# Kernel optimization log

Hardware: AMD Instinct MI355X
Metric: run time of the kernel (lower is better)

The kernel has to match this reference:

```python
import jax, jax.numpy as jnp
import numpy as np

N, E = 100000, 1600000
NFEAT, H2, H3, H4, NCLASS = 512, 256, 256, 128, 16


def setup_inputs() -> dict:
    key = jax.random.key(0)
    ks = jax.random.split(key, 12)
    def glorot(k, shape):
        fan_in = shape[0]
        return jax.random.normal(k, shape, dtype=jnp.float32) * (1.0 / np.sqrt(fan_in))
    return {
        "x": jax.random.normal(ks[0], (N, NFEAT), dtype=jnp.float32),
        "edge_row": jax.random.randint(ks[1], (E,), 0, N, dtype=jnp.int32),
        "edge_col": jax.random.randint(ks[2], (E,), 0, N, dtype=jnp.int32),
        # positive weights ~ normalized adjacency values (scale ~1/avg_degree)
        "edge_val": jax.random.uniform(ks[3], (E,), dtype=jnp.float32) * (1.0 / 16.0),
        "W1": glorot(ks[4], (NFEAT, H2)), "b1": jnp.zeros((H2,), jnp.float32),
        "W2": glorot(ks[5], (H2, H3)),   "b2": jnp.zeros((H3,), jnp.float32),
        "W3": glorot(ks[6], (H3, H4)),   "b3": jnp.zeros((H4,), jnp.float32),
        "Wd": glorot(ks[7], (H4, NCLASS)), "bd": jnp.zeros((NCLASS,), jnp.float32),
    }


def reference(x, edge_row, edge_col, edge_val, W1, b1, W2, b2, W3, b3, Wd, bd):
    n = x.shape[0]

    def spmm(h):
        # adj @ h with adj in COO form: out[row] += val * h[col]
        return jax.ops.segment_sum(edge_val[:, None] * h[edge_col], edge_row, num_segments=n)

    # gc1 -> relu -> (dropout is identity in eval) -> gc2 -> relu -> gc3 -> relu -> dense
    h = jax.nn.relu(spmm(x @ W1) + b1)
    h = jax.nn.relu(spmm(h @ W2) + b2)
    h = jax.nn.relu(spmm(h @ W3) + b3)
    return h @ Wd + bd
```

## Files before the change

### kernel.cpp

```cpp
#include <hip/hip_runtime.h>
#include <hip/hip_bf16.h>
#include <cstdint>
#include <cstddef>

#define NFEAT 512
#define H2 256
#define H3 256
#define H4 128
#define NCLASS 16

typedef __attribute__((ext_vector_type(8))) short short8;
typedef __attribute__((ext_vector_type(4))) float f32x4;
typedef __attribute__((ext_vector_type(4))) unsigned short ushort4v;
typedef __attribute__((ext_vector_type(4))) _Float16 half4v;
typedef __attribute__((ext_vector_type(2))) _Float16 half2v;

#define AS1 __attribute__((address_space(1)))
#define AS3 __attribute__((address_space(3)))

__device__ inline unsigned short f2bf_rne(float x) {
    unsigned int u = __builtin_bit_cast(unsigned int, x);
    unsigned int r = (u + 0x7FFFu + ((u >> 16) & 1u)) >> 16;
    return (unsigned short)r;
}
__device__ inline float bf2f(unsigned short h) {
    return __builtin_bit_cast(float, (unsigned int)h << 16);
}

template <int VM> __device__ __forceinline__ void vm_wait() {
    asm volatile("s_waitcnt vmcnt(%0)" :: "n"(VM) : "memory");
}
__device__ __forceinline__ void lgkm0() {
    asm volatile("s_waitcnt lgkmcnt(0)" ::: "memory");
}

__global__ void k_hist(const int* __restrict__ er, int* __restrict__ cnt, int E) {
    for (int e = blockIdx.x * blockDim.x + threadIdx.x; e < E; e += gridDim.x * blockDim.x)
        atomicAdd(&cnt[er[e]], 1);
}

__global__ void k_scan1(const int* __restrict__ cnt, int* __restrict__ ex,
                        int* __restrict__ bsum, int n) {
    __shared__ int s[256];
    int i = blockIdx.x * 256 + threadIdx.x;
    int v = (i < n) ? cnt[i] : 0;
    s[threadIdx.x] = v;
    __syncthreads();
    #pragma unroll
    for (int off = 1; off < 256; off <<= 1) {
        int t = (threadIdx.x >= (unsigned)off) ? s[threadIdx.x - off] : 0;
        __syncthreads();
        s[threadIdx.x] += t;
        __syncthreads();
    }
    if (i < n) ex[i] = s[threadIdx.x] - v;
    if (threadIdx.x == 255) bsum[blockIdx.x] = s[255];
}

__global__ void k_scan2(int* __restrict__ bsum, int nb) {
    __shared__ int s[512];
    int v = ((int)threadIdx.x < nb) ? bsum[threadIdx.x] : 0;
    s[threadIdx.x] = v;
    __syncthreads();
    #pragma unroll
    for (int off = 1; off < 512; off <<= 1) {
        int t = (threadIdx.x >= (unsigned)off) ? s[threadIdx.x - off] : 0;
        __syncthreads();
        s[threadIdx.x] += t;
        __syncthreads();
    }
    if ((int)threadIdx.x < nb) bsum[threadIdx.x] = s[threadIdx.x] - v;
}

__global__ void k_scan3(int* __restrict__ rp, int* __restrict__ ofs,
                        const int* __restrict__ bsum, const int* __restrict__ cnt,
                        int n) {
    int i = blockIdx.x * 256 + threadIdx.x;
    if (i < n) {
        int v = rp[i] + bsum[blockIdx.x];
        rp[i] = v;
        ofs[i] = v;
        if (i == n - 1) rp[n] = v + cnt[i];
    }
}

__global__ void k_scatter(const int* __restrict__ er, const int* __restrict__ ec,
                          const float* __restrict__ ev, int* __restrict__ ofs,
                          int2* __restrict__ ev2, int E) {
    for (int e = blockIdx.x * blockDim.x + threadIdx.x; e < E; e += gridDim.x * blockDim.x) {
        int r = er[e];
        int p = atomicAdd(&ofs[r], 1);
        ev2[p] = make_int2(ec[e], __builtin_bit_cast(int, ev[e]));
    }
}

__global__ __launch_bounds__(256)
void k_packb(const float* __restrict__ W, unsigned short* __restrict__ hi,
             unsigned short* __restrict__ lo, int K, int M) {
    int idx = blockIdx.x * 256 + threadIdx.x;
    int NT = K >> 5;
    int total = (M >> 4) * NT * 64;
    if (idx >= total) return;
    int l = idx & 63;
    int t = (idx >> 6) % NT;
    int cg = idx / (NT << 6);
    int col = cg * 16 + (l & 15);
    int k0 = t * 32 + (l >> 4) * 8;
    short8 h8, l8;
    #pragma unroll
    for (int j = 0; j < 8; ++j) {
        float x = W[(size_t)(k0 + j) * M + col];
        unsigned short h = f2bf_rne(x);
        h8[j] = (short)h;
        l8[j] = (short)f2bf_rne(x - bf2f(h));
    }
    *(short8*)&hi[(size_t)idx * 8] = h8;
    *(short8*)&lo[(size_t)idx * 8] = l8;
}

__global__ __launch_bounds__(256, 3)
void k_gemm1c(const float* __restrict__ X, const unsigned short* __restrict__ Bh,
              const unsigned short* __restrict__ Bl, _Float16* __restrict__ C16, const int N) {
    constexpr int K = 512, M = 256, NT = K / 32;
    __shared__ char smem[24576];
    float* sX = (float*)smem;
    const int tid = threadIdx.x;
    const int lane = tid & 63;
    const int w = tid >> 6;
    const int lm = lane & 15, lk = lane >> 4;
    const int row0 = blockIdx.x * 64;
    const int col0 = w * 64;

    const int kseg = (lane & 7) ^ ((lane >> 3) & 7);
    const int r0 = min(row0 + w * 16 + (lane >> 3), N - 1);
    const int r1 = min(row0 + w * 16 + 8 + (lane >> 3), N - 1);
    const size_t ga0 = (size_t)r0 * K + kseg * 4;
    const size_t ga1 = (size_t)r1 * K + kseg * 4;

    const unsigned short* bfh = Bh + ((size_t)(w * 4) * NT) * 512 + lane * 8;
    const unsigned short* bfl = Bl + ((size_t)(w * 4) * NT) * 512 + lane * 8;

    f32x4 acc[4][4];
    #pragma unroll
    for (int i = 0; i < 4; ++i)
        #pragma unroll
        for (int j = 0; j < 4; ++j) acc[i][j] = (f32x4){0.f, 0.f, 0.f, 0.f};

    auto stage = [&](int bi, int kk) {
        __builtin_amdgcn_global_load_lds((const AS1 void*)(X + ga0 + kk),
                                         (AS3 void*)(sX + bi * 2048 + w * 512), 16, 0, 0);
        __builtin_amdgcn_global_load_lds((const AS1 void*)(X + ga1 + kk),
                                         (AS3 void*)(sX + bi * 2048 + w * 512 + 256), 16, 0, 0);
    };

    stage(0, 0); stage(1, 32); stage(2, 64);

    short8 bhf[4], blf[4];
    #pragma unroll
    for (int nf = 0; nf < 4; ++nf) {
        const size_t o = (size_t)nf * NT * 512;
        bhf[nf] = *(const short8*)(bfh + o);
        blf[nf] = *(const short8*)(bfl + o);
    }

    const int u0 = ((2 * lk) ^ (lm & 7)) * 4;
    const int u1 = ((2 * lk + 1) ^ (lm & 7)) * 4;
    int bi = 0;

#define G1_BODY(T, VM)                                                          \
    {                                                                           \
        vm_wait<VM>();                                                          \
        __builtin_amdgcn_s_barrier();                                           \
        __builtin_amdgcn_sched_barrier(0);                                      \
        short8 bhn[4], bln[4];                                                  \
        _Pragma("unroll")                                                       \
        for (int nf = 0; nf < 4; ++nf) { bhn[nf] = bhf[nf]; bln[nf] = blf[nf]; }\
        if ((T) + 1 < NT) {                                                     \
            _Pragma("unroll")                                                   \
            for (int nf = 0; nf < 4; ++nf) {                                    \
                const size_t o = ((size_t)nf * NT + (T) + 1) * 512;             \
                bhn[nf] = *(const short8*)(bfh + o);                            \
                bln[nf] = *(const short8*)(bfl + o);                            \
            }                                                                   \
        }                                                                       \
        __builtin_amdgcn_sched_barrier(0);                                      \
        _Pragma("unroll")                                                       \
        for (int mf = 0; mf < 4; ++mf) {                                        \
            const float* ab = sX + bi * 2048 + (mf * 16 + lm) * 32;             \
            f32x4 p0 = *(const f32x4*)(ab + u0);                                \
            f32x4 p1 = *(const f32x4*)(ab + u1);                                \
            float vv[8] = {p0.x, p0.y, p0.z, p0.w, p1.x, p1.y, p1.z, p1.w};     \
            short8 ah, al;                                                      \
            _Pragma("unroll")                                                   \
            for (int j = 0; j < 8; ++j) {                                       \
                unsigned int uu = __builtin_bit_cast(unsigned int, vv[j]);      \
                ah[j] = (short)(uu >> 16);                                      \
                float hi_ = __builtin_bit_cast(float, uu & 0xFFFF0000u);        \
                al[j] = (short)f2bf_rne(vv[j] - hi_);                           \
            }                                                                   \
            _Pragma("unroll")                                                   \
            for (int nf = 0; nf < 4; ++nf) {                                    \
                acc[mf][nf] = __builtin_amdgcn_mfma_f32_16x16x32_bf16(ah, bhf[nf], acc[mf][nf], 0, 0, 0); \
                acc[mf][nf] = __builtin_amdgcn_mfma_f32_16x16x32_bf16(ah, blf[nf], acc[mf][nf], 0, 0, 0); \
                acc[mf][nf] = __builtin_amdgcn_mfma_f32_16x16x32_bf16(al, bhf[nf], acc[mf][nf], 0, 0, 0); \
            }                                                                   \
        }                                                                       \
        lgkm0();                                                                \
        __builtin_amdgcn_sched_barrier(0);                                      \
        __builtin_amdgcn_s_barrier();                                           \
        if ((T) + 3 < NT) stage(bi, ((T) + 3) * 32);                            \
        _Pragma("unroll")                                                       \
        for (int nf = 0; nf < 4; ++nf) { bhf[nf] = bhn[nf]; blf[nf] = bln[nf]; }\
        bi = bi + 1; if (bi == 3) bi = 0;                                       \
    }

    for (int t = 0; t < NT - 2; ++t) G1_BODY(t, 12);
    G1_BODY(NT - 2, 10);
    G1_BODY(NT - 1, 8);
#undef G1_BODY

    float* sc = (float*)smem;
    #pragma unroll
    for (int mf = 0; mf < 4; ++mf) {
        __syncthreads();
        #pragma unroll
        for (int nf = 0; nf < 4; ++nf)
            #pragma unroll
            for (int r = 0; r < 4; ++r) {
                const int rl = lk * 4 + r;
                const int col = col0 + nf * 16 + lm;
                sc[rl * M + (col ^ (lk << 3))] = acc[mf][nf][r];
            }
        __syncthreads();
        #pragma unroll
        for (int i = 0; i < 4; ++i) {
            const int idx = i * 256 + tid;
            const int rl = idx >> 6, u = idx & 63;
            const int grow = row0 + mf * 16 + rl;
            if (grow < N) {
                f32x4 v = *(const f32x4*)&sc[rl * M + ((u * 4) ^ (((rl >> 2) & 3) << 3))];
                half4v h;
                h[0] = (_Float16)v[0]; h[1] = (_Float16)v[1];
                h[2] = (_Float16)v[2]; h[3] = (_Float16)v[3];
                *(half4v*)&C16[(size_t)grow * M + u * 4] = h;
            }
        }
    }
}

template <int K, int NFW>
__global__ __launch_bounds__(256, 3)
void k_gemm_btc(const unsigned short* __restrict__ Ah, const unsigned short* __restrict__ Al,
                const unsigned short* __restrict__ Bh, const unsigned short* __restrict__ Bl,
                _Float16* __restrict__ C16, const int N) {
    constexpr int M = 64 * NFW;
    constexpr int NT = K / 32;
    constexpr int UPR = 16 * NFW;
    __shared__ char smem[24576];
    unsigned short* sAh = (unsigned short*)smem;
    unsigned short* sAl = sAh + 6144;
    const int tid = threadIdx.x;
    const int lane = tid & 63;
    const int w = tid >> 6;
    const int lm = lane & 15, lk = lane >> 4;
    const int row0 = blockIdx.x * 64;
    const int col0 = w * (16 * NFW);

    const int kseg = (lane & 3) ^ ((lane >> 2) & 3);
    const int gr = min(row0 + w * 16 + (lane >> 2), N - 1);
    const size_t ga = (size_t)gr * K + kseg * 8;

    const int aoff = lm * 32 + ((lk ^ (lm & 3)) * 8);

    const unsigned short* bfh = Bh + ((size_t)(w * NFW) * NT) * 512 + lane * 8;
    const unsigned short* bfl = Bl + ((size_t)(w * NFW) * NT) * 512 + lane * 8;

    f32x4 acc[4][NFW];
    #pragma unroll
    for (int i = 0; i < 4; ++i)
        #pragma unroll
        for (int j = 0; j < NFW; ++j) acc[i][j] = (f32x4){0.f, 0.f, 0.f, 0.f};

    auto stage = [&](int bi, int kk) {
        __builtin_amdgcn_global_load_lds((const AS1 void*)(Ah + ga + kk),
                                         (AS3 void*)(sAh + bi * 2048 + w * 512), 16, 0, 0);
        __builtin_amdgcn_global_load_lds((const AS1 void*)(Al + ga + kk),
                                         (AS3 void*)(sAl + bi * 2048 + w * 512), 16, 0, 0);
    };

    stage(0, 0); stage(1, 32); stage(2, 64);

    short8 bhf[NFW], blf[NFW];
    #pragma unroll
    for (int nf = 0; nf < NFW; ++nf) {
        const size_t o = (size_t)nf * NT * 512;
        bhf[nf] = *(const short8*)(bfh + o);
        blf[nf] = *(const short8*)(bfl + o);
    }

    int bi = 0;

#define GBT_BODY(T, VM)                                                         \
    {                                                                           \
        vm_wait<VM>();                                                          \
        __builtin_amdgcn_s_barrier();                                           \
        __builtin_amdgcn_sched_barrier(0);                                      \
        short8 bhn[NFW], bln[NFW];                                              \
        _Pragma("unroll")                                                       \
        for (int nf = 0; nf < NFW; ++nf) { bhn[nf] = bhf[nf]; bln[nf] = blf[nf]; } \
        if ((T) + 1 < NT) {                                                     \
            _Pragma("unroll")                                                   \
            for (int nf = 0; nf < NFW; ++nf) {                                  \
                const size_t o = ((size_t)nf * NT + (T) + 1) * 512;             \
                bhn[nf] = *(const short8*)(bfh + o);                            \
                bln[nf] = *(const short8*)(bfl + o);                            \
            }                                                                   \
        }                                                                       \
        __builtin_amdgcn_sched_barrier(0);                                      \
        _Pragma("unroll")                                                       \
        for (int mf = 0; mf < 4; ++mf) {                                        \
            short8 ah = *(const short8*)&sAh[bi * 2048 + aoff + mf * 512];      \
            short8 al = *(const short8*)&sAl[bi * 2048 + aoff + mf * 512];      \
            _Pragma("unroll")                                                   \
            for (int nf = 0; nf < NFW; ++nf) {                                  \
                acc[mf][nf] = __builtin_amdgcn_mfma_f32_16x16x32_bf16(ah, bhf[nf], acc[mf][nf], 0, 0, 0); \
                acc[mf][nf] = __builtin_amdgcn_mfma_f32_16x16x32_bf16(ah, blf[nf], acc[mf][nf], 0, 0, 0); \
                acc[mf][nf] = __builtin_amdgcn_mfma_f32_16x16x32_bf16(al, bhf[nf], acc[mf][nf], 0, 0, 0); \
            }                                                                   \
        }                                                                       \
        lgkm0();                                                                \
        __builtin_amdgcn_sched_barrier(0);                                      \
        __builtin_amdgcn_s_barrier();                                           \
        if ((T) + 3 < NT) stage(bi, ((T) + 3) * 32);                            \
        _Pragma("unroll")                                                       \
        for (int nf = 0; nf < NFW; ++nf) { bhf[nf] = bhn[nf]; blf[nf] = bln[nf]; } \
        bi = bi + 1; if (bi == 3) bi = 0;                                       \
    }

    for (int t = 0; t < NT - 2; ++t) GBT_BODY(t, 2 * NFW + 4);
    GBT_BODY(NT - 2, 2 * NFW + 2);
    GBT_BODY(NT - 1, 2 * NFW);
#undef GBT_BODY

    float* sc = (float*)smem;
    #pragma unroll
    for (int mf = 0; mf < 4; ++mf) {
        __syncthreads();
        #pragma unroll
        for (int nf = 0; nf < NFW; ++nf)
            #pragma unroll
            for (int r = 0; r < 4; ++r) {
                const int rl = lk * 4 + r;
                const int col = col0 + nf * 16 + lm;
                sc[rl * M + (col ^ (lk << 3))] = acc[mf][nf][r];
            }
        __syncthreads();
        #pragma unroll
        for (int i = 0; i < (16 * UPR) / 256; ++i) {
            const int idx = i * 256 + tid;
            const int rl = idx / UPR, u = idx % UPR;
            const int grow = row0 + mf * 16 + rl;
            if (grow < N) {
                f32x4 v = *(const f32x4*)&sc[rl * M + ((u * 4) ^ (((rl >> 2) & 3) << 3))];
                half4v h;
                h[0] = (_Float16)v[0]; h[1] = (_Float16)v[1];
                h[2] = (_Float16)v[2]; h[3] = (_Float16)v[3];
                *(half4v*)&C16[(size_t)grow * M + u * 4] = h;
            }
        }
    }
}

__global__ __launch_bounds__(256)
void k_spmm256f(const int* __restrict__ rp, const int2* __restrict__ ev2,
                const _Float16* __restrict__ in16, const float* __restrict__ bias,
                unsigned short* __restrict__ oh, unsigned short* __restrict__ ol, int N) {
    const int lane = threadIdx.x & 63;
    int r = __builtin_amdgcn_readfirstlane(blockIdx.x * 4 + (threadIdx.x >> 6));
    if (r >= N) return;
    const int e0 = __builtin_amdgcn_readfirstlane(rp[r]);
    const int e1 = __builtin_amdgcn_readfirstlane(rp[r + 1]);
    f32x4 acc = {0.f, 0.f, 0.f, 0.f};
    const _Float16* base = in16 + lane * 4;

    #pragma unroll 4
    for (int e = e0; e < e1; ++e) {
        int2 p = ev2[e];
        half4v hv = *(const half4v*)(base + (size_t)p.x * 256);
        float val = __builtin_bit_cast(float, p.y);
        acc[0] = fmaf(val, (float)hv[0], acc[0]);
        acc[1] = fmaf(val, (float)hv[1], acc[1]);
        acc[2] = fmaf(val, (float)hv[2], acc[2]);
        acc[3] = fmaf(val, (float)hv[3], acc[3]);
    }

    f32x4 bv = *(const f32x4*)&bias[lane * 4];
    ushort4v h, l;
    #pragma unroll
    for (int j = 0; j < 4; ++j) {
        float o = fmaxf(acc[j] + bv[j], 0.f);
        unsigned short hh = f2bf_rne(o);
        h[j] = hh;
        l[j] = f2bf_rne(o - bf2f(hh));
    }
    *(ushort4v*)&oh[(size_t)r * 256 + lane * 4] = h;
    *(ushort4v*)&ol[(size_t)r * 256 + lane * 4] = l;
}

__global__ __launch_bounds__(256)
void k_spmm128f(const int* __restrict__ rp, const int2* __restrict__ ev2,
                const _Float16* __restrict__ in16, const float* __restrict__ b3,
                const float* __restrict__ Wd, const float* __restrict__ bd,
                float* __restrict__ out, int N) {
    __shared__ float Ws[H4 * NCLASS];
    __shared__ float hrow[4][H4];
    {
        int i = threadIdx.x * 8;
        *(f32x4*)&Ws[i] = *(const f32x4*)&Wd[i];
        *(f32x4*)&Ws[i + 4] = *(const f32x4*)&Wd[i + 4];
    }
    __syncthreads();

    const int lane = threadIdx.x & 63;
    const int w = threadIdx.x >> 6;
    int r = __builtin_amdgcn_readfirstlane(blockIdx.x * 4 + w);
    if (r >= N) return;
    const int e0 = __builtin_amdgcn_readfirstlane(rp[r]);
    const int e1 = __builtin_amdgcn_readfirstlane(rp[r + 1]);
    float a0 = 0.f, a1 = 0.f;
    const _Float16* base = in16 + lane * 2;

    #pragma unroll 4
    for (int e = e0; e < e1; ++e) {
        int2 p = ev2[e];
        half2v hv = *(const half2v*)(base + (size_t)p.x * 128);
        float v = __builtin_bit_cast(float, p.y);
        a0 = fmaf(v, (float)hv[0], a0);
        a1 = fmaf(v, (float)hv[1], a1);
    }

    float2 hb;
    hb.x = fmaxf(a0 + b3[lane * 2 + 0], 0.f);
    hb.y = fmaxf(a1 + b3[lane * 2 + 1], 0.f);
    *(float2*)&hrow[w][lane * 2] = hb;

    const int c = lane & 15, q = lane >> 4;
    float s = 0.f;
    #pragma unroll
    for (int k = q * 32; k < q * 32 + 32; ++k)
        s = fmaf(hrow[w][k], Ws[k * NCLASS + c], s);
    s += __shfl_xor(s, 16);
    s += __shfl_xor(s, 32);
    if (lane < 16) out[(size_t)r * NCLASS + lane] = s + bd[lane];
}

extern "C" void kernel_launch(void* const* d_in, const int* in_sizes, int n_in,
                              void* d_out, int out_size, void* d_ws, size_t ws_size,
                              hipStream_t stream) {
    const float* x  = (const float*)d_in[0];
    const int*   er = (const int*)d_in[1];
    const int*   ec = (const int*)d_in[2];
    const float* ev = (const float*)d_in[3];
    const float* W1 = (const float*)d_in[4];
    const float* b1 = (const float*)d_in[5];
    const float* W2 = (const float*)d_in[6];
    const float* b2 = (const float*)d_in[7];
    const float* W3 = (const float*)d_in[8];
    const float* b3 = (const float*)d_in[9];
    const float* Wd = (const float*)d_in[10];
    const float* bd = (const float*)d_in[11];
    float* out = (float*)d_out;

    const int N = in_sizes[0] / NFEAT;
    const int E = in_sizes[1];

    char* w = (char*)d_ws;
    auto alloc = [&](size_t bytes) { char* p = w; w += (bytes + 255) & ~(size_t)255; return p; };
    _Float16* C16 = (_Float16*)alloc((size_t)N * 256 * 2);
    unsigned short* hh = (unsigned short*)alloc((size_t)N * 256 * 2);
    unsigned short* hl = (unsigned short*)alloc((size_t)N * 256 * 2);
    int* cnt  = (int*)alloc((size_t)N * 4);
    int* rp   = (int*)alloc((size_t)(N + 1) * 4);
    int* ofs  = (int*)alloc((size_t)N * 4);
    int2* ev2 = (int2*)alloc((size_t)E * 8);
    int* bsum = (int*)alloc(4096);
    unsigned short* W1h = (unsigned short*)alloc((size_t)NFEAT * H2 * 2);
    unsigned short* W1l = (unsigned short*)alloc((size_t)NFEAT * H2 * 2);
    unsigned short* W2h = (unsigned short*)alloc((size_t)H2 * H3 * 2);
    unsigned short* W2l = (unsigned short*)alloc((size_t)H2 * H3 * 2);
    unsigned short* W3h = (unsigned short*)alloc((size_t)H3 * H4 * 2);
    unsigned short* W3l = (unsigned short*)alloc((size_t)H3 * H4 * 2);

    const int nb = (N + 255) / 256;

    hipMemsetAsync(cnt, 0, (size_t)N * 4, stream);
    k_hist<<<1024, 256, 0, stream>>>(er, cnt, E);
    k_scan1<<<nb, 256, 0, stream>>>(cnt, rp, bsum, N);
    k_scan2<<<1, 512, 0, stream>>>(bsum, nb);
    k_scan3<<<nb, 256, 0, stream>>>(rp, ofs, bsum, cnt, N);
    k_scatter<<<1024, 256, 0, stream>>>(er, ec, ev, ofs, ev2, E);

    k_packb<<<(NFEAT * H2 / 8 + 255) / 256, 256, 0, stream>>>(W1, W1h, W1l, NFEAT, H2);
    k_packb<<<(H2 * H3 / 8 + 255) / 256, 256, 0, stream>>>(W2, W2h, W2l, H2, H3);
    k_packb<<<(H3 * H4 / 8 + 255) / 256, 256, 0, stream>>>(W3, W3h, W3l, H3, H4);

    const int rgrid = (N + 63) / 64;
    const int sgrid = (N + 3) / 4;

    k_gemm1c<<<rgrid, 256, 0, stream>>>(x, W1h, W1l, C16, N);
    k_spmm256f<<<sgrid, 256, 0, stream>>>(rp, ev2, C16, b1, hh, hl, N);

    k_gemm_btc<H2, 4><<<rgrid, 256, 0, stream>>>(hh, hl, W2h, W2l, C16, N);
    k_spmm256f<<<sgrid, 256, 0, stream>>>(rp, ev2, C16, b2, hh, hl, N);

    k_gemm_btc<H3, 2><<<rgrid, 256, 0, stream>>>(hh, hl, W3h, W3l, C16, N);
    k_spmm128f<<<sgrid, 256, 0, stream>>>(rp, ev2, C16, b3, Wd, bd, out, N);
}
```

Measured before the change: 691.5 us.

## Replace direct COO-to-CSR scatter with two-pass bucketed placement

The single random scatter of edges into CSR order is split into two passes. The first buckets edges by 256-row block into a temporary buffer, with the local row packed into the high bits of the column index. The second pass has one workgroup per block place its edges into final CSR positions. The aim is to make the final writes and atomics local to a small region, improving cache behaviour, at the cost of an extra E-sized buffer, an extra pass and heavy atomic contention on the per-bucket counters. The packing assumes column indices fit in 17 bits.

```diff
diff --git a/kernel.cpp b/kernel.cpp
--- a/kernel.cpp
+++ b/kernel.cpp
@@ -84,13 +84,34 @@
     }
 }
 
-__global__ void k_scatter(const int* __restrict__ er, const int* __restrict__ ec,
-                          const float* __restrict__ ev, int* __restrict__ ofs,
-                          int2* __restrict__ ev2, int E) {
+__global__ void k_binit(const int* __restrict__ rp, int* __restrict__ bofs, int nbk) {
+    int i = blockIdx.x * 256 + threadIdx.x;
+    if (i < nbk) bofs[i] = rp[i * 256];
+}
+
+__global__ void k_bucket(const int* __restrict__ er, const int* __restrict__ ec,
+                         const float* __restrict__ ev, int* __restrict__ bofs,
+                         int2* __restrict__ tmp, int E) {
     for (int e = blockIdx.x * blockDim.x + threadIdx.x; e < E; e += gridDim.x * blockDim.x) {
         int r = er[e];
-        int p = atomicAdd(&ofs[r], 1);
-        ev2[p] = make_int2(ec[e], __builtin_bit_cast(int, ev[e]));
+        int p = atomicAdd(&bofs[r >> 8], 1);
+        tmp[p] = make_int2(ec[e] | ((r & 255) << 17), __builtin_bit_cast(int, ev[e]));
+    }
+}
+
+__global__ __launch_bounds__(256)
+void k_place(const int2* __restrict__ tmp, const int* __restrict__ rp,
+             int* __restrict__ ofs, int2* __restrict__ ev2, int N) {
+    const int b = blockIdx.x;
+    const int row0 = b * 256;
+    const int beg = rp[row0];
+    const int end = rp[min(row0 + 256, N)];
+    for (int e = beg + threadIdx.x; e < end; e += 256) {
+        int2 t = tmp[e];
+        int row = row0 + ((t.x >> 17) & 255);
+        int col = t.x & 0x1FFFF;
+        int pos = atomicAdd(&ofs[row], 1);
+        ev2[pos] = make_int2(col, t.y);
     }
 }
 
@@ -483,7 +504,9 @@
     int* rp   = (int*)alloc((size_t)(N + 1) * 4);
     int* ofs  = (int*)alloc((size_t)N * 4);
     int2* ev2 = (int2*)alloc((size_t)E * 8);
+    int2* tmp = (int2*)alloc((size_t)E * 8);
     int* bsum = (int*)alloc(4096);
+    int* bofs = (int*)alloc(((size_t)N / 256 + 2) * 4);
     unsigned short* W1h = (unsigned short*)alloc((size_t)NFEAT * H2 * 2);
     unsigned short* W1l = (unsigned short*)alloc((size_t)NFEAT * H2 * 2);
     unsigned short* W2h = (unsigned short*)alloc((size_t)H2 * H3 * 2);
@@ -498,7 +521,9 @@
     k_scan1<<<nb, 256, 0, stream>>>(cnt, rp, bsum, N);
     k_scan2<<<1, 512, 0, stream>>>(bsum, nb);
     k_scan3<<<nb, 256, 0, stream>>>(rp, ofs, bsum, cnt, N);
-    k_scatter<<<1024, 256, 0, stream>>>(er, ec, ev, ofs, ev2, E);
+    k_binit<<<(nb + 255) / 256, 256, 0, stream>>>(rp, bofs, nb);
+    k_bucket<<<2048, 256, 0, stream>>>(er, ec, ev, bofs, tmp, E);
+    k_place<<<nb, 256, 0, stream>>>(tmp, rp, ofs, ev2, N);
 
     k_packb<<<(NFEAT * H2 / 8 + 255) / 256, 256, 0, stream>>>(W1, W1h, W1l, NFEAT, H2);
     k_packb<<<(H2 * H3 / 8 + 255) / 256, 256, 0, stream>>>(W2, W2h, W2l, H2, H3);
```

Result: slower. 1.182 ms (+71.0%).
